# Kernel optimization log

Hardware: AMD Instinct MI355X
Metric: run time of the kernel (lower is better)

Reference implementation:

```python
import jax, jax.numpy as jnp
import numpy as np

K = 3          # kernel_size
G = 8          # group
C = 256        # in_channel
EPS_BN = 1e-5
EPS_SGE = 1e-5


def setup_inputs() -> dict:
    key = jax.random.key(0)
    ks = jax.random.split(key, 6)
    x = jax.random.normal(ks[0], (8, C, 96, 96), dtype=jnp.float32)
    fan_out = (G * K * K) * K * K  # out_channels * kh * kw (kaiming fan_out)
    conv_weight = jax.random.normal(ks[1], (G * K * K, C, K, K), dtype=jnp.float32) * np.float32(np.sqrt(2.0 / fan_out))
    bn_gamma = 1.0 + 0.1 * jax.random.normal(ks[2], (G * K * K,), dtype=jnp.float32)
    bn_beta = 0.1 * jax.random.normal(ks[3], (G * K * K,), dtype=jnp.float32)
    sge_weight = 0.1 * jax.random.normal(ks[4], (1, G, 1, 1), dtype=jnp.float32)
    sge_bias = 1.0 + 0.1 * jax.random.normal(ks[5], (1, G, 1, 1), dtype=jnp.float32)
    return {"x": x, "sge_weight": sge_weight, "sge_bias": sge_bias,
            "conv_weight": conv_weight, "bn_gamma": bn_gamma, "bn_beta": bn_beta}


def _reflect_pad(x, p):
    return jnp.pad(x, ((0, 0), (0, 0), (p, p), (p, p)), mode="reflect")


def _sge(x, weight, bias):
    # SpatialGroupEnhance
    b, c, h, w = x.shape
    xg = x.reshape(b * G, c // G, h, w)
    gap = xg.mean(axis=(2, 3), keepdims=True)        # AdaptiveAvgPool2d(1)
    xn = (xg * gap).sum(axis=1, keepdims=True)       # (b*G,1,h,w)
    t = xn.reshape(b * G, h * w)
    t = t - t.mean(axis=1, keepdims=True)
    std = jnp.std(t, axis=1, ddof=1, keepdims=True) + EPS_SGE  # torch .std() is unbiased
    t = (t / std).reshape(b, G, h, w)
    t = t * weight + bias
    gate = jax.nn.sigmoid(t.reshape(b * G, 1, h, w))
    return (xg * gate).reshape(b, c, h, w)


def _pasa(x, conv_weight, bn_gamma, bn_beta):
    # Downsample_PASA_group_softmax (stride=1)
    n, c, h, w = x.shape
    xp = _reflect_pad(x, K // 2)
    s = jax.lax.conv_general_dilated(xp, conv_weight, (1, 1), "VALID",
                                     dimension_numbers=("NCHW", "OIHW", "NCHW"))
    # BatchNorm2d in training mode: batch statistics over (N,H,W), biased var
    mean = s.mean(axis=(0, 2, 3))
    var = s.var(axis=(0, 2, 3))
    s = (s - mean[None, :, None, None]) * jax.lax.rsqrt(var + EPS_BN)[None, :, None, None]
    s = s * bn_gamma[None, :, None, None] + bn_beta[None, :, None, None]
    s = jax.nn.softmax(s, axis=1)                    # over the G*K*K channels
    # channels are (group, k*k) group-major -> (n, G, 1, K*K, H*W)
    return s.reshape(n, G, K * K, h * w)[:, :, None, :, :]


def _unfold(xp, h, w):
    # xp already padded; returns (b, c, K*K, h, w) with torch F.unfold ordering
    return jnp.stack([xp[:, :, i:i + h, j:j + w]
                      for i in range(K) for j in range(K)], axis=2)


def reference(x, sge_weight, sge_bias, conv_weight, bn_gamma, bn_beta):
    n, c, h, w = x.shape
    sigma = _pasa(x, conv_weight, bn_gamma, bn_beta)       # (n, G, 1, KK, HW)
    xe = _sge(x, sge_weight, sge_bias)
    patches = _unfold(_reflect_pad(xe, K // 2), h, w)      # (n, c, KK, h, w)
    patches = patches.reshape(n, G, c // G, K * K, h * w)  # split c group-major
    out = (patches * sigma).sum(axis=3)                    # reduce over K*K taps
    return out.reshape(n, c, h, w)
```

## Files before the change

kernel.cpp:

```cpp
#include <hip/hip_runtime.h>
#include <hip/hip_bf16.h>

#define B_  8
#define C_  256
#define H_  96
#define W_  96
#define G_  8
#define CPG 32
#define KK  9
#define O_  72
#define HW  9216
#define NPX 73728

typedef short bf16x8 __attribute__((ext_vector_type(8)));
typedef float f32x4 __attribute__((ext_vector_type(4)));

__device__ __forceinline__ unsigned short f2bf(float f) {
    union { float f; unsigned u; } v; v.f = f;
    unsigned r = v.u + 0x7fffu + ((v.u >> 16) & 1u);
    return (unsigned short)(r >> 16);
}
__device__ __forceinline__ float bf2f(unsigned short h) {
    union { float f; unsigned u; } v; v.u = ((unsigned)h) << 16;
    return v.f;
}

__global__ __launch_bounds__(256) void bprep_kernel(const float* __restrict__ w,
                                                    unsigned short* __restrict__ bpk) {
    int idx = blockIdx.x * 256 + threadIdx.x;
    if (idx >= 368640) return;
    int tix2 = idx / 5120;
    int r = idx - tix2 * 5120;
    int fi = r >> 9;
    int p = fi / 5, nt = fi - p * 5;
    int li = r & 511;
    int l = li >> 3, j = li & 7;
    int tap = tix2 >> 3, cblk = tix2 & 7;
    int o = nt * 16 + (l & 15);
    int c = cblk * 32 + ((l >> 4) << 3) + j;
    unsigned short val = 0;
    if (o < O_) {
        float wv = w[((size_t)o * C_ + c) * KK + tap];
        unsigned short h = f2bf(wv);
        val = (p == 0) ? h : f2bf(wv - bf2f(h));
    }
    bpk[idx] = val;
}

__global__ __launch_bounds__(256) void xn_kernel(const float* __restrict__ x,
                                                 const float* __restrict__ gap,
                                                 float* __restrict__ xng,
                                                 float* __restrict__ sge_stats) {
    int blk = blockIdx.x;
    int bg = blk / 36, chunk = blk % 36;
    int b = bg >> 3, g = bg & 7;
    int p = chunk * 256 + threadIdx.x;
    const float* xbase = x + ((size_t)b * C_ + g * CPG) * HW + p;
    const float* gp = gap + b * C_ + g * CPG;
    float v = 0.f;
    #pragma unroll
    for (int ch = 0; ch < CPG; ch++) v += xbase[(size_t)ch * HW] * gp[ch];
    v *= (1.f / (float)HW);
    xng[(size_t)bg * HW + p] = v;
    float v1 = v, v2 = v * v;
    #pragma unroll
    for (int m = 32; m >= 1; m >>= 1) {
        v1 += __shfl_xor(v1, m, 64);
        v2 += __shfl_xor(v2, m, 64);
    }
    __shared__ float r1[4], r2[4];
    int wid = threadIdx.x >> 6;
    if ((threadIdx.x & 63) == 0) { r1[wid] = v1; r2[wid] = v2; }
    __syncthreads();
    if (threadIdx.x == 0) {
        atomicAdd(&sge_stats[bg * 2 + 0], r1[0] + r1[1] + r1[2] + r1[3]);
        atomicAdd(&sge_stats[bg * 2 + 1], r2[0] + r2[1] + r2[2] + r2[3]);
    }
}

#define STAGE_LOAD(CH) do {                                                      \
    const float* p0_ = sb0 + (size_t)(CH) * 32 * HW;                             \
    const float* p1_ = p0_ + HW;                                                 \
    _Pragma("unroll")                                                            \
    for (int m2 = 0; m2 < 6; m2++) {                                             \
        a0[m2] = *(const f32x4*)(p0_ + 4 * m2);                                  \
        a1[m2] = *(const f32x4*)(p1_ + 4 * m2);                                  \
    }                                                                            \
} while (0)

#define PACK_HL(F0, F1, HI, LO) do {                                             \
    unsigned b0_ = __builtin_bit_cast(unsigned, (F0));                           \
    unsigned b1_ = __builtin_bit_cast(unsigned, (F1));                           \
    HI = __builtin_amdgcn_perm(b1_, b0_, 0x07060302u);                           \
    float h0_ = __builtin_bit_cast(float, b0_ & 0xffff0000u);                    \
    float h1_ = __builtin_bit_cast(float, b1_ & 0xffff0000u);                    \
    LO = __builtin_amdgcn_perm(__builtin_bit_cast(unsigned, (F1) - h1_),         \
                               __builtin_bit_cast(unsigned, (F0) - h0_),         \
                               0x07060302u);                                     \
} while (0)

#define STAGE_WRITE(CH) do {                                                     \
    _Pragma("unroll")                                                            \
    for (int m2 = 0; m2 < 6; m2++)                                               \
        _Pragma("unroll")                                                        \
        for (int e = 0; e < 4; e++) {                                            \
            int col = sq * 24 + 1 + m2 * 4 + e;                                  \
            unsigned hi_, lo_;                                                   \
            PACK_HL(a0[m2][e], a1[m2][e], hi_, lo_);                             \
            int row = (rbase + col) ^ par;                                       \
            int off = row * 16 + ((spHi ^ ((col >> 1) & 3)) << 2) + spLo;        \
            xsH[off] = hi_; xsL[off] = lo_;                                      \
        }                                                                        \
    if (sq == 0 || sq == 3) {                                                    \
        float f0_ = (sq == 0) ? a0[0][1] : a0[5][2];                             \
        float f1_ = (sq == 0) ? a1[0][1] : a1[5][2];                             \
        int col = (sq == 0) ? 0 : 97;                                            \
        unsigned hi_, lo_;                                                       \
        PACK_HL(f0_, f1_, hi_, lo_);                                             \
        int row = (rbase + col) ^ par;                                           \
        int off = row * 16 + ((spHi ^ ((col >> 1) & 3)) << 2) + spLo;            \
        xsH[off] = hi_; xsL[off] = lo_;                                          \
    }                                                                            \
    {                   \
        float s0_ = 0.f, s1_ = 0.f;                                              \
        if (srr == 1 || srr == 2) {                                              \
            _Pragma("unroll")                                                    \
            for (int m2 = 0; m2 < 6; m2++) {                                     \
                s0_ += a0[m2][0] + a0[m2][1] + a0[m2][2] + a0[m2][3];            \
                s1_ += a1[m2][0] + a1[m2][1] + a1[m2][2] + a1[m2][3];            \
            }                                                                    \
        }                                                                        \
        s0_ += __shfl_xor(s0_, 48, 64);                                          \
        s1_ += __shfl_xor(s1_, 48, 64);                                          \
        if (srr == 1) {                                                          \
            gapP[(CH) * 128 + sq * 32 + 2 * sp]     = s0_;                       \
            gapP[(CH) * 128 + sq * 32 + 2 * sp + 1] = s1_;                       \
        }                                                                        \
    }                                                                            \
} while (0)

__global__ __launch_bounds__(256, 2) void conv_kernel(const float* __restrict__ x,
                                                      const unsigned short* __restrict__ bpk,
                                                      float* __restrict__ sA,
                                                      float* __restrict__ sB,
                                                      float* __restrict__ gap) {
    __shared__ unsigned xsH[4 * 98 * 16];
    __shared__ unsigned xsL[4 * 98 * 16];
    __shared__ f32x4 blsv[2][640];
    __shared__ float gapP[512];
    int phys = blockIdx.x;
    int blk = (phys & 7) * 96 + (phys >> 3);
    int kh = blk & 1;
    int np = blk >> 1;
    int n = np / 48, pair = np % 48;
    int i0 = pair * 2;
    int t = threadIdx.x;
    int l = t & 63, wave = t >> 6;
    int rw = wave & 1, mh = wave >> 1;
    int l15 = l & 15, lg = l >> 4;
    int colb = mh * 48 + l15;
    int khb = kh * 4;
    const float* xb = x + (size_t)n * C_ * HW + (size_t)kh * 128 * HW;
    float* sOut = kh ? sB : sA;

    int sp = t & 15, srr = (t >> 4) & 3, sq = wave;
    int sri = i0 - 1 + srr;
    if (sri < 0) sri = 1; else if (sri > 95) sri = 94;
    const float* sb0 = xb + (size_t)(2 * sp) * HW + sri * W_ + sq * 24;
    int spHi = sp >> 2, spLo = sp & 3;
    int rbase = srr * 98, par = srr & 1;

    f32x4 acc[3][5];
    #pragma unroll
    for (int m = 0; m < 3; m++)
        #pragma unroll
        for (int nt = 0; nt < 5; nt++)
            #pragma unroll
            for (int e = 0; e < 4; e++) acc[m][nt][e] = 0.f;

    f32x4 a0[6], a1[6];

    {
        const f32x4* srcB = (const f32x4*)(bpk + (size_t)khb * 5120);
        f32x4 b0 = srcB[t], b1 = srcB[t + 256], b2;
        if (t < 128) b2 = srcB[t + 512];
        blsv[0][t] = b0; blsv[0][t + 256] = b1;
        if (t < 128) blsv[0][t + 512] = b2;
        STAGE_LOAD(0);
        STAGE_WRITE(0);
    }
    __syncthreads();

    for (int ch = 0; ch < 4; ch++) {
        #pragma unroll 1
        for (int tap = 0; tap < 9; tap++) {
            int g = ch * 9 + tap;
            int buf = g & 1;
            int dr = tap / 3, dc = tap - dr * 3;
            const unsigned short* bb = (const unsigned short*)&blsv[buf][0];
            bf16x8 bh[5], blo[5];
            #pragma unroll
            for (int nt = 0; nt < 5; nt++) {
                bh[nt]  = *(const bf16x8*)(bb + nt * 512 + (l << 3));
                blo[nt] = *(const bf16x8*)(bb + (5 + nt) * 512 + (l << 3));
            }
            int rr = rw + dr;
            int rpar = rr & 1, rb = rr * 98;
            int cs = ((colb + dc) >> 1) & 3;
            int sl = (lg ^ cs) << 2;
            bf16x8 ah[3], al[3];
            #pragma unroll
            for (int m = 0; m < 3; m++) {
                int row = (rb + colb + m * 16 + dc) ^ rpar;
                ah[m] = *(const bf16x8*)&xsH[row * 16 + sl];
                al[m] = *(const bf16x8*)&xsL[row * 16 + sl];
            }
            f32x4 pb0, pb1, pb2;
            bool hasNext = (g < 35);
            if (hasNext) {
                int tix2n = (tap < 8) ? (tap + 1) * 8 + khb + ch : khb + ch + 1;
                const f32x4* srcB = (const f32x4*)(bpk + (size_t)tix2n * 5120);
                pb0 = srcB[t]; pb1 = srcB[t + 256];
                if (t < 128) pb2 = srcB[t + 512];
            }
            if (tap == 7 && ch < 3) STAGE_LOAD(ch + 1);
            #pragma unroll
            for (int m = 0; m < 3; m++)
                #pragma unroll
                for (int nt = 0; nt < 5; nt++) {
                    acc[m][nt] = __builtin_amdgcn_mfma_f32_16x16x32_bf16(ah[m], bh[nt],  acc[m][nt], 0, 0, 0);
                    acc[m][nt] = __builtin_amdgcn_mfma_f32_16x16x32_bf16(ah[m], blo[nt], acc[m][nt], 0, 0, 0);
                    acc[m][nt] = __builtin_amdgcn_mfma_f32_16x16x32_bf16(al[m], bh[nt],  acc[m][nt], 0, 0, 0);
                }
            if (hasNext) {
                blsv[buf ^ 1][t] = pb0; blsv[buf ^ 1][t + 256] = pb1;
                if (t < 128) blsv[buf ^ 1][t + 512] = pb2;
                __syncthreads();
            }
        }
        if (ch < 3) {
            STAGE_WRITE(ch + 1);
            __syncthreads();
        }
    }

    int i = i0 + rw;
    #pragma unroll
    for (int nt = 0; nt < 5; nt++) {
        int o = nt * 16 + l15;
        if (o < O_) {
            #pragma unroll
            for (int m = 0; m < 3; m++) {
                int px = mh * 48 + m * 16 + (lg << 2);
                *(f32x4*)(sOut + ((size_t)(n * O_ + o) * H_ + i) * W_ + px) = acc[m][nt];
            }
        }
    }
    __syncthreads();
    if (t < 128) {
        int chf = t >> 5, cc = t & 31;
        float v = gapP[chf * 128 + cc] + gapP[chf * 128 + 32 + cc]
                + gapP[chf * 128 + 64 + cc] + gapP[chf * 128 + 96 + cc];
        atomicAdd(&gap[n * C_ + kh * 128 + chf * 32 + cc], v);
    }
}

__global__ __launch_bounds__(256) void bnstats_kernel(float* __restrict__ sA,
                                                      const float* __restrict__ sB,
                                                      float* __restrict__ bn_stats) {
    int blk = blockIdx.x;
    int o = blk / B_, nn = blk % B_;
    size_t base = ((size_t)nn * O_ + o) * HW;
    f32x4* pa = (f32x4*)(sA + base);
    const f32x4* pb = (const f32x4*)(sB + base);
    float s1 = 0.f, s2 = 0.f;
    for (int idx = threadIdx.x; idx < HW / 4; idx += 256) {
        f32x4 v = pa[idx] + pb[idx];
        pa[idx] = v;
        s1 += v[0] + v[1] + v[2] + v[3];
        s2 += v[0] * v[0] + v[1] * v[1] + v[2] * v[2] + v[3] * v[3];
    }
    #pragma unroll
    for (int m = 32; m >= 1; m >>= 1) {
        s1 += __shfl_xor(s1, m, 64);
        s2 += __shfl_xor(s2, m, 64);
    }
    __shared__ float r1[4], r2[4];
    int wid = threadIdx.x >> 6;
    if ((threadIdx.x & 63) == 0) { r1[wid] = s1; r2[wid] = s2; }
    __syncthreads();
    if (threadIdx.x == 0) {
        atomicAdd(&bn_stats[o * 2 + 0], r1[0] + r1[1] + r1[2] + r1[3]);
        atomicAdd(&bn_stats[o * 2 + 1], r2[0] + r2[1] + r2[2] + r2[3]);
    }
}

__global__ __launch_bounds__(256, 2) void out_kernel(const float* __restrict__ x,
                                                     const float* __restrict__ s,
                                                     const float* __restrict__ bn_stats,
                                                     const float* __restrict__ gamma,
                                                     const float* __restrict__ beta,
                                                     const float* __restrict__ xn,
                                                     const float* __restrict__ sstats,
                                                     const float* __restrict__ sw,
                                                     const float* __restrict__ sb,
                                                     float* __restrict__ out) {
    int blk = blockIdx.x;
    int n = blk / H_, i = blk % H_;
    int t = threadIdx.x;
    __shared__ float sg[O_][W_];
    __shared__ float rden[W_];
    __shared__ float gt[G_][3][100];

    int r0 = i - 1; if (r0 < 0) r0 = 1;
    int r2 = i + 1; if (r2 > 95) r2 = 94;
    int rows[3] = { r0, i, r2 };

    for (int idx = t; idx < G_ * 3 * 98; idx += 256) {
        int g = idx / (3 * 98), rem = idx % (3 * 98);
        int r = rem / 98, col = rem % 98;
        int gcol = col - 1;
        if (gcol < 0) gcol = 1; else if (gcol > 95) gcol = 94;
        float v = xn[((size_t)(n * G_ + g)) * HW + rows[r] * W_ + gcol];
        int bg = n * G_ + g;
        float sum = sstats[bg * 2], sumsq = sstats[bg * 2 + 1];
        float mean = sum * (1.f / (float)HW);
        float var = (sumsq - sum * mean) * (1.f / (float)(HW - 1));
        var = fmaxf(var, 0.f);
        float sd = sqrtf(var) + 1e-5f;
        float tv = (v - mean) / sd * sw[g] + sb[g];
        gt[g][r][col] = 1.f / (1.f + expf(-tv));
    }
    const float inv = 1.f / (float)NPX;
    for (int idx = t; idx < O_ * W_; idx += 256) {
        int o = idx / W_, j = idx % W_;
        float sum = bn_stats[o * 2], ssq = bn_stats[o * 2 + 1];
        float mean = sum * inv;
        float var = ssq * inv - mean * mean;
        float sc = rsqrtf(var + 1e-5f) * gamma[o];
        float val = (s[((size_t)(n * O_ + o) * H_ + i) * W_ + j] - mean) * sc + beta[o];
        sg[o][j] = expf(val);
    }
    __syncthreads();
    if (t < W_) {
        float d = 0.f;
        #pragma unroll
        for (int o = 0; o < O_; o++) d += sg[o][t];
        rden[t] = 1.f / d;
    }
    __syncthreads();

    const float* xb = x + (size_t)n * C_ * HW;
    for (int idx = t; idx < C_ * 24; idx += 256) {
        int c = idx / 24, jq = idx % 24;
        int j0 = jq * 4;
        int g = c >> 5;
        const float* xc = xb + (size_t)c * HW;
        float prod[3][6];
        #pragma unroll
        for (int r = 0; r < 3; r++) {
            const float* xr = xc + rows[r] * W_;
            float4 m = *(const float4*)(xr + j0);
            float lft = (j0 == 0)  ? xr[1]  : xr[j0 - 1];
            float rgt = (j0 == 92) ? xr[94] : xr[j0 + 4];
            const float* gr = &gt[g][r][0];
            float4 gm = *(const float4*)(gr + j0);
            float g4 = gr[j0 + 4], g5 = gr[j0 + 5];
            prod[r][0] = lft * gm.x;
            prod[r][1] = m.x * gm.y;
            prod[r][2] = m.y * gm.z;
            prod[r][3] = m.z * gm.w;
            prod[r][4] = m.w * g4;
            prod[r][5] = rgt * g5;
        }
        float o0 = 0.f, o1 = 0.f, o2 = 0.f, o3 = 0.f;
        #pragma unroll
        for (int r = 0; r < 3; r++)
            #pragma unroll
            for (int dx = 0; dx < 3; dx++) {
                float4 sv = *(const float4*)&sg[g * 9 + r * 3 + dx][j0];
                o0 += prod[r][0 + dx] * sv.x;
                o1 += prod[r][1 + dx] * sv.y;
                o2 += prod[r][2 + dx] * sv.z;
                o3 += prod[r][3 + dx] * sv.w;
            }
        float4 rd = *(const float4*)&rden[j0];
        float4 res;
        res.x = o0 * rd.x; res.y = o1 * rd.y; res.z = o2 * rd.z; res.w = o3 * rd.w;
        *(float4*)(out + ((size_t)(n * C_ + c) * H_ + i) * W_ + j0) = res;
    }
}

extern "C" void kernel_launch(void* const* d_in, const int* in_sizes, int n_in,
                              void* d_out, int out_size, void* d_ws, size_t ws_size,
                              hipStream_t stream) {
    const float* x      = (const float*)d_in[0];
    const float* sge_w  = (const float*)d_in[1];
    const float* sge_b  = (const float*)d_in[2];
    const float* conv_w = (const float*)d_in[3];
    const float* gamma  = (const float*)d_in[4];
    const float* beta   = (const float*)d_in[5];
    float* out = (float*)d_out;
    float* ws = (float*)d_ws;

    float* sge_stats = ws;
    float* bn_stats  = ws + 128;
    float* gap       = ws + 272;
    float* xng       = ws + 2320;
    unsigned short* bpk = (unsigned short*)(ws + 592144);
    float* sA        = ws + 776464;
    float* sB = (float*)d_out;

    hipMemsetAsync(d_ws, 0, 2320 * sizeof(float), stream);
    hipLaunchKernelGGL(bprep_kernel,   dim3(1440),        dim3(256), 0, stream, conv_w, bpk);
    hipLaunchKernelGGL(conv_kernel,    dim3(768),         dim3(256), 0, stream, x, bpk, sA, sB, gap);
    hipLaunchKernelGGL(xn_kernel,      dim3(B_ * G_ * 36),dim3(256), 0, stream, x, gap, xng, sge_stats);
    hipLaunchKernelGGL(bnstats_kernel, dim3(O_ * B_),     dim3(256), 0, stream, sA, sB, bn_stats);
    hipLaunchKernelGGL(out_kernel,     dim3(B_ * H_),     dim3(256), 0, stream,
                       x, sA, bn_stats, gamma, beta, xng, sge_stats, sge_w, sge_b, out);
}
```

Baseline: 197.6 us.

## Load conv weight fragments directly into registers with two-tap prefetch, drop LDS staging

Weight B fragments are now read from global memory straight into two register sets that alternate, fetched two taps ahead, instead of being staged through a double-buffered LDS array. This removes the per-tap LDS write, LDS read and __syncthreads, and the tap loop is fully unrolled per channel chunk. The cost is 20 extra bf16x8 registers per thread under launch_bounds(256,2), which risks spills, plus redundant global loads across waves that L2 has to serve.

```diff
diff --git a/kernel.cpp b/kernel.cpp
--- a/kernel.cpp
+++ b/kernel.cpp
@@ -139,6 +139,40 @@
     }                                                                            \
 } while (0)
 
+#define BLOAD(P, TIX2) do {                                                      \
+    const unsigned short* bp_ = bpk + (size_t)(TIX2) * 5120 + (l << 3);          \
+    _Pragma("unroll")                                                            \
+    for (int q = 0; q < 10; q++) P[q] = *(const bf16x8*)(bp_ + q * 512);         \
+} while (0)
+
+#define TAPB(TAP, P) do {                                                        \
+    int rr_ = rw + (TAP) / 3;                                                    \
+    int rpar_ = rr_ & 1, rb_ = rr_ * 98;                                         \
+    int cs_ = ((colb + (TAP) % 3) >> 1) & 3;                                     \
+    int sl_ = (lg ^ cs_) << 2;                                                   \
+    bf16x8 ah[3], al[3];                                                         \
+    _Pragma("unroll")                                                            \
+    for (int m = 0; m < 3; m++) {                                                \
+        int row = (rb_ + colb + m * 16 + (TAP) % 3) ^ rpar_;                     \
+        ah[m] = *(const bf16x8*)&xsH[row * 16 + sl_];                            \
+        al[m] = *(const bf16x8*)&xsL[row * 16 + sl_];                            \
+    }                                                                            \
+    if ((TAP) == 7 && chv < 3) STAGE_LOAD(chv + 1);                              \
+    _Pragma("unroll")                                                            \
+    for (int m = 0; m < 3; m++)                                                  \
+        _Pragma("unroll")                                                        \
+        for (int nt = 0; nt < 5; nt++) {                                         \
+            acc[m][nt] = __builtin_amdgcn_mfma_f32_16x16x32_bf16(ah[m], P[nt],     acc[m][nt], 0, 0, 0); \
+            acc[m][nt] = __builtin_amdgcn_mfma_f32_16x16x32_bf16(ah[m], P[5 + nt], acc[m][nt], 0, 0, 0); \
+            acc[m][nt] = __builtin_amdgcn_mfma_f32_16x16x32_bf16(al[m], P[nt],     acc[m][nt], 0, 0, 0); \
+        }                                                                        \
+    if (chv * 9 + (TAP) <= 33) {            \
+        int tp2_ = ((TAP) < 7) ? (TAP) + 2 : (TAP) - 7;                          \
+        int ch2_ = ((TAP) < 7) ? chv : chv + 1;                                  \
+        BLOAD(P, tp2_ * 8 + khb + ch2_);                                         \
+    }                                                                            \
+} while (0)
+
 __global__ __launch_bounds__(256, 2) void conv_kernel(const float* __restrict__ x,
                                                       const unsigned short* __restrict__ bpk,
                                                       float* __restrict__ sA,
@@ -146,7 +180,6 @@
                                                       float* __restrict__ gap) {
     __shared__ unsigned xsH[4 * 98 * 16];
     __shared__ unsigned xsL[4 * 98 * 16];
-    __shared__ f32x4 blsv[2][640];
     __shared__ float gapP[512];
     int phys = blockIdx.x;
     int blk = (phys & 7) * 96 + (phys >> 3);
@@ -179,68 +212,35 @@
             for (int e = 0; e < 4; e++) acc[m][nt][e] = 0.f;
 
     f32x4 a0[6], a1[6];
+    bf16x8 bA[10], bB[10];
 
     {
-        const f32x4* srcB = (const f32x4*)(bpk + (size_t)khb * 5120);
-        f32x4 b0 = srcB[t], b1 = srcB[t + 256], b2;
-        if (t < 128) b2 = srcB[t + 512];
-        blsv[0][t] = b0; blsv[0][t + 256] = b1;
-        if (t < 128) blsv[0][t + 512] = b2;
         STAGE_LOAD(0);
         STAGE_WRITE(0);
-    }
-    __syncthreads();
-
-    for (int ch = 0; ch < 4; ch++) {
-        #pragma unroll 1
-        for (int tap = 0; tap < 9; tap++) {
-            int g = ch * 9 + tap;
-            int buf = g & 1;
-            int dr = tap / 3, dc = tap - dr * 3;
-            const unsigned short* bb = (const unsigned short*)&blsv[buf][0];
-            bf16x8 bh[5], blo[5];
-            #pragma unroll
-            for (int nt = 0; nt < 5; nt++) {
-                bh[nt]  = *(const bf16x8*)(bb + nt * 512 + (l << 3));
-                blo[nt] = *(const bf16x8*)(bb + (5 + nt) * 512 + (l << 3));
-            }
-            int rr = rw + dr;
-            int rpar = rr & 1, rb = rr * 98;
-            int cs = ((colb + dc) >> 1) & 3;
-            int sl = (lg ^ cs) << 2;
-            bf16x8 ah[3], al[3];
-            #pragma unroll
-            for (int m = 0; m < 3; m++) {
-                int row = (rb + colb + m * 16 + dc) ^ rpar;
-                ah[m] = *(const bf16x8*)&xsH[row * 16 + sl];
-                al[m] = *(const bf16x8*)&xsL[row * 16 + sl];
-            }
-            f32x4 pb0, pb1, pb2;
-            bool hasNext = (g < 35);
-            if (hasNext) {
-                int tix2n = (tap < 8) ? (tap + 1) * 8 + khb + ch : khb + ch + 1;
-                const f32x4* srcB = (const f32x4*)(bpk + (size_t)tix2n * 5120);
-                pb0 = srcB[t]; pb1 = srcB[t + 256];
-                if (t < 128) pb2 = srcB[t + 512];
-            }
-            if (tap == 7 && ch < 3) STAGE_LOAD(ch + 1);
-            #pragma unroll
-            for (int m = 0; m < 3; m++)
-                #pragma unroll
-                for (int nt = 0; nt < 5; nt++) {
-                    acc[m][nt] = __builtin_amdgcn_mfma_f32_16x16x32_bf16(ah[m], bh[nt],  acc[m][nt], 0, 0, 0);
-                    acc[m][nt] = __builtin_amdgcn_mfma_f32_16x16x32_bf16(ah[m], blo[nt], acc[m][nt], 0, 0, 0);
-                    acc[m][nt] = __builtin_amdgcn_mfma_f32_16x16x32_bf16(al[m], bh[nt],  acc[m][nt], 0, 0, 0);
-                }
-            if (hasNext) {
-                blsv[buf ^ 1][t] = pb0; blsv[buf ^ 1][t + 256] = pb1;
-                if (t < 128) blsv[buf ^ 1][t + 512] = pb2;
+        BLOAD(bA, khb);
+        BLOAD(bB, 8 + khb);
+    }
+    __syncthreads();
+
+    #pragma unroll 1
+    for (int chp = 0; chp < 2; chp++) {
+        {
+            int chv = chp * 2;
+            TAPB(0, bA); TAPB(1, bB); TAPB(2, bA); TAPB(3, bB); TAPB(4, bA);
+            TAPB(5, bB); TAPB(6, bA); TAPB(7, bB); TAPB(8, bA);
+            __syncthreads();
+            STAGE_WRITE(chv + 1);
+            __syncthreads();
+        }
+        {
+            int chv = chp * 2 + 1;
+            TAPB(0, bB); TAPB(1, bA); TAPB(2, bB); TAPB(3, bA); TAPB(4, bB);
+            TAPB(5, bA); TAPB(6, bB); TAPB(7, bA); TAPB(8, bB);
+            if (chv < 3) {
+                __syncthreads();
+                STAGE_WRITE(chv + 1);
                 __syncthreads();
             }
-        }
-        if (ch < 3) {
-            STAGE_WRITE(ch + 1);
-            __syncthreads();
         }
     }
 
```

After: 312.9 us. +58.4%, slower.
